# Kernel optimization log

Measured on AMD Instinct MI355X. Metric: run time of the kernel, lower is better.

## Reference

```python
import jax, jax.numpy as jnp
import numpy as np


def _ln(x, g, b, eps=1e-6):
    m = jnp.mean(x, axis=-1, keepdims=True)
    v = jnp.var(x, axis=-1, keepdims=True)
    return (x - m) * jax.lax.rsqrt(v + eps) * g + b


def setup_inputs():
    key = jax.random.key(0)
    ks = jax.random.split(key, 16)
    B, Hs, Ws, D = 2, 48, 48, 768
    heads, P = 6, 4
    L = Hs * Ws                # feat tokens (single level, 1/16 scale)
    N = 21 * (Hs * Ws // 4)    # query tokens: 16n + 4n + n multi-scale layout
    hidden = int(D * 0.25)
    s = 0.02
    return {
        "query": jax.random.normal(ks[0], (B, N, D), jnp.float32),
        "reference_points": jax.random.uniform(ks[1], (B, N, 1, 2), jnp.float32),
        "feat": jax.random.normal(ks[2], (B, L, D), jnp.float32),
        "spatial_shapes": jnp.array([[Hs, Ws]], jnp.int32),
        "level_start_index": jnp.array([0], jnp.int32),
        "H": Hs, "W": Ws,
        "qn_g": jnp.ones((D,), jnp.float32), "qn_b": jnp.zeros((D,), jnp.float32),
        "fn_g": jnp.ones((D,), jnp.float32), "fn_b": jnp.zeros((D,), jnp.float32),
        "Wv": jax.random.normal(ks[3], (D, D), jnp.float32) * s, "bv": jnp.zeros((D,), jnp.float32),
        "Woff": jax.random.normal(ks[4], (D, heads * P * 2), jnp.float32) * s,
        "boff": jax.random.normal(ks[5], (heads * P * 2,), jnp.float32) * s,
        "Wattn": jax.random.normal(ks[6], (D, heads * P), jnp.float32) * s,
        "battn": jnp.zeros((heads * P,), jnp.float32),
        "Wo": jax.random.normal(ks[7], (D, D), jnp.float32) * s, "bo": jnp.zeros((D,), jnp.float32),
        "ffn_g": jnp.ones((D,), jnp.float32), "ffn_b": jnp.zeros((D,), jnp.float32),
        "W1": jax.random.normal(ks[8], (D, hidden), jnp.float32) * s, "b1": jnp.zeros((hidden,), jnp.float32),
        "dw_w": jax.random.normal(ks[9], (hidden, 1, 3, 3), jnp.float32) * s, "dw_b": jnp.zeros((hidden,), jnp.float32),
        "W2": jax.random.normal(ks[10], (hidden, D), jnp.float32) * s, "b2": jnp.zeros((D,), jnp.float32),
    }


def reference(query, reference_points, feat, spatial_shapes, level_start_index, H, W,
              qn_g, qn_b, fn_g, fn_b, Wv, bv, Woff, boff, Wattn, battn, Wo, bo,
              ffn_g, ffn_b, W1, b1, dw_w, dw_b, W2, b2):
    B, N, D = query.shape
    heads, P = 6, 4
    dh = D // heads
    hidden = W1.shape[1]
    # ---- MSDeformAttn (single level) ----
    qn = _ln(query, qn_g, qn_b)
    fn = _ln(feat, fn_g, fn_b)
    value = (fn @ Wv + bv).reshape(B, -1, heads, dh)           # (B,L,h,dh)
    off = (qn @ Woff + boff).reshape(B, N, heads, 1, P, 2)
    aw = jax.nn.softmax((qn @ Wattn + battn).reshape(B, N, heads, P), axis=-1)
    # offset normalizer = [W_l, H_l]
    norm = jnp.stack([spatial_shapes[..., 1], spatial_shapes[..., 0]], -1).astype(qn.dtype)
    loc = reference_points[:, :, None, :, None, :] + off / norm[None, None, None, :, None, :]
    loc = loc[:, :, :, 0]  # (B,N,heads,P,2) single level
    # grid_sample bilinear, align_corners=False, zero padding
    x = loc[..., 0] * W - 0.5
    y = loc[..., 1] * H - 0.5
    x0 = jnp.floor(x); y0 = jnp.floor(y)
    wx = x - x0; wy = y - y0
    x0 = x0.astype(jnp.int32); y0 = y0.astype(jnp.int32)
    value_t = value.transpose(0, 2, 1, 3)  # (B,heads,L,dh)

    def corner(xi, yi, w):
        valid = (xi >= 0) & (xi < W) & (yi >= 0) & (yi < H)
        idx = jnp.clip(yi, 0, H - 1) * W + jnp.clip(xi, 0, W - 1)
        idx = idx.transpose(0, 2, 1, 3).reshape(B, heads, N * P)
        v = jnp.take_along_axis(value_t, idx[..., None], axis=2)  # (B,h,N*P,dh)
        wm = jnp.where(valid, w, 0.0).transpose(0, 2, 1, 3).reshape(B, heads, N * P)
        return v * wm[..., None]

    sampled = (corner(x0, y0, (1 - wx) * (1 - wy)) + corner(x0 + 1, y0, wx * (1 - wy))
               + corner(x0, y0 + 1, (1 - wx) * wy) + corner(x0 + 1, y0 + 1, wx * wy))
    sampled = sampled.reshape(B, heads, N, P, dh)
    attn = jnp.einsum('bhnpd,bnhp->bnhd', sampled, aw).reshape(B, N, D) @ Wo + bo
    query = query + attn
    # ---- ConvFFN (hidden=dim*cffn_ratio, multi-scale DWConv) ----
    h = _ln(query, ffn_g, ffn_b) @ W1 + b1
    n = N // 21

    def dw(t, hh, ww):
        img = t.transpose(0, 2, 1).reshape(B, hidden, hh, ww)
        out = jax.lax.conv_general_dilated(img, dw_w, (1, 1), 'SAME', feature_group_count=hidden)
        return (out + dw_b[None, :, None, None]).reshape(B, hidden, hh * ww).transpose(0, 2, 1)

    h = jnp.concatenate([dw(h[:, :16 * n], 2 * H, 2 * W),
                         dw(h[:, 16 * n:20 * n], H, W),
                         dw(h[:, 20 * n:], H // 2, W // 2)], axis=1)
    h = jax.nn.gelu(h, approximate=False)
    return query + (h @ W2 + b2)
```

## Files before the change

### kernel.cpp

```cpp
#include <hip/hip_runtime.h>
#include <math.h>

#define BB 2
#define NN 12096
#define LL 2304
#define DD 768
#define HID 192
#define HS 48
#define WS 48

typedef unsigned short u16;
typedef unsigned int u32;
typedef __attribute__((ext_vector_type(8))) __bf16 bf16x8;
typedef __attribute__((ext_vector_type(4))) float f32x4;

__device__ __forceinline__ u16 f2bf(float f) {
  u32 x = __builtin_bit_cast(u32, f);
  u32 r = (x + 0x7fffu + ((x >> 16) & 1u)) >> 16;
  return (u16)r;
}
__device__ __forceinline__ float bf2f(u16 u) {
  u32 x = ((u32)u) << 16;
  return __builtin_bit_cast(float, x);
}

template <typename T>
__device__ __forceinline__ void ln_row4(const T* xr, const float* g, const float* bta, u16* yr, int t) {
  float v0, v1, v2, v3;
  if constexpr (sizeof(T) == 2) {
    ushort4 u = *(const ushort4*)(xr + 4 * t);
    v0 = bf2f(u.x); v1 = bf2f(u.y); v2 = bf2f(u.z); v3 = bf2f(u.w);
  } else {
    float4 f = *(const float4*)(xr + 4 * t);
    v0 = f.x; v1 = f.y; v2 = f.z; v3 = f.w;
  }
  float s = v0 + v1 + v2 + v3;
  float s2 = v0 * v0 + v1 * v1 + v2 * v2 + v3 * v3;
#pragma unroll
  for (int off = 32; off; off >>= 1) {
    s += __shfl_down(s, off, 64);
    s2 += __shfl_down(s2, off, 64);
  }
  __shared__ float red[6];
  __shared__ float mv[2];
  int wave = t >> 6, lane = t & 63;
  if (lane == 0) { red[wave] = s; red[3 + wave] = s2; }
  __syncthreads();
  if (t == 0) {
    float ts = red[0] + red[1] + red[2];
    float ts2 = red[3] + red[4] + red[5];
    float m = ts * (1.f / DD);
    float var = ts2 * (1.f / DD) - m * m;
    mv[0] = m;
    mv[1] = rsqrtf(var + 1e-6f);
  }
  __syncthreads();
  float m = mv[0], rs = mv[1];
  float4 gv = *(const float4*)(g + 4 * t);
  float4 bv = *(const float4*)(bta + 4 * t);
  ushort4 o;
  o.x = f2bf((v0 - m) * rs * gv.x + bv.x);
  o.y = f2bf((v1 - m) * rs * gv.y + bv.y);
  o.z = f2bf((v2 - m) * rs * gv.z + bv.z);
  o.w = f2bf((v3 - m) * rs * gv.w + bv.w);
  *(ushort4*)(yr + 4 * t) = o;
}

template <typename T>
__global__ __launch_bounds__(192) void ln_kernel(const T* __restrict__ x,
                                                 const float* __restrict__ g,
                                                 const float* __restrict__ bta,
                                                 u16* __restrict__ y) {
  size_t row = blockIdx.x;
  ln_row4<T>(x + row * DD, g, bta, y + row * DD, threadIdx.x);
}

__global__ __launch_bounds__(192) void ln_dual_kernel(const float* __restrict__ xq,
                                                      const float* __restrict__ gq,
                                                      const float* __restrict__ bq,
                                                      u16* __restrict__ yq,
                                                      const float* __restrict__ xf,
                                                      const float* __restrict__ gf,
                                                      const float* __restrict__ bf_,
                                                      u16* __restrict__ yf,
                                                      int Mq) {
  size_t row = blockIdx.x;
  if (row < (size_t)Mq)
    ln_row4<float>(xq + row * DD, gq, bq, yq + row * DD, threadIdx.x);
  else {
    size_t r = row - Mq;
    ln_row4<float>(xf + r * DD, gf, bf_, yf + r * DD, threadIdx.x);
  }
}

template <int BM, int BN, int WM, int WN, int RES, int OUT, int NTSW>
__global__ __launch_bounds__(256, 4) void gemm_bf16(const u16* __restrict__ A,
                                                    const u16* __restrict__ Bt,
                                                    const float* __restrict__ bias,
                                                    const void* __restrict__ res,
                                                    void* __restrict__ Cv,
                                                    int M, int N, int K) {
  constexpr int PM = BM / WM, PN = BN / WN;
  constexpr int FM = PM / 16, FN = PN / 16;
  constexpr int ASEG = BM / 32;
  constexpr int BSEG = BN / 32;
  int bx, by;
  if (NTSW > 0) {
    int flat = blockIdx.x;
    int x = flat & 7, gidx = flat >> 3;
    bx = gidx % NTSW;
    int mg = gidx / NTSW;
    by = mg * 8 + x;
    if (by * BM >= M) return;
  } else {
    bx = blockIdx.x;
    by = blockIdx.y;
  }
  __shared__ u16 As[BM * 64];
  __shared__ u16 Bs[BN * 64];
  int tid = threadIdx.x;
  int w = tid >> 6, lane = tid & 63;
  int rw = w / WN, cw = w % WN;
  int m0 = by * BM, n0 = bx * BN;

  f32x4 acc[FM][FN];
#pragma unroll
  for (int i = 0; i < FM; ++i)
#pragma unroll
    for (int j = 0; j < FN; ++j) acc[i][j] = (f32x4){0.f, 0.f, 0.f, 0.f};

  int lr = lane >> 3;
  int lq = lane & 7;
  int qg = lq ^ lr;
  int l15 = lane & 15, quad = lane >> 4;

  for (int k0 = 0; k0 < K; k0 += 64) {
#pragma unroll
    for (int i = 0; i < ASEG; ++i) {
      int s = w * ASEG + i;
      int row = s * 8 + lr;
      const u16* gp = A + (size_t)(m0 + row) * K + k0 + qg * 8;
      __builtin_amdgcn_global_load_lds(
          (const __attribute__((address_space(1))) void*)gp,
          (__attribute__((address_space(3))) void*)&As[s * 512], 16, 0, 0);
    }
#pragma unroll
    for (int i = 0; i < BSEG; ++i) {
      int s = w * BSEG + i;
      int row = s * 8 + lr;
      const u16* gp = Bt + (size_t)(n0 + row) * K + k0 + qg * 8;
      __builtin_amdgcn_global_load_lds(
          (const __attribute__((address_space(1))) void*)gp,
          (__attribute__((address_space(3))) void*)&Bs[s * 512], 16, 0, 0);
    }
    __syncthreads();
#pragma unroll
    for (int s2 = 0; s2 < 2; ++s2) {
      bf16x8 af[FM], bfr[FN];
#pragma unroll
      for (int mt = 0; mt < FM; ++mt) {
        int rm = rw * PM + mt * 16 + l15;
        int ch = (s2 * 4 + quad) ^ (rm & 7);
        af[mt] = *(const bf16x8*)&As[rm * 64 + ch * 8];
      }
#pragma unroll
      for (int nt = 0; nt < FN; ++nt) {
        int rn = cw * PN + nt * 16 + l15;
        int ch = (s2 * 4 + quad) ^ (rn & 7);
        bfr[nt] = *(const bf16x8*)&Bs[rn * 64 + ch * 8];
      }
#pragma unroll
      for (int mt = 0; mt < FM; ++mt)
#pragma unroll
        for (int nt = 0; nt < FN; ++nt)
          acc[mt][nt] = __builtin_amdgcn_mfma_f32_16x16x32_bf16(af[mt], bfr[nt], acc[mt][nt], 0, 0, 0);
    }
    __syncthreads();
  }

#pragma unroll
  for (int mt = 0; mt < FM; ++mt) {
    int m = m0 + rw * PM + mt * 16 + quad * 4;
#pragma unroll
    for (int nt = 0; nt < FN; ++nt) {
      int n = n0 + cw * PN + nt * 16 + l15;
      float bsv = bias[n];
#pragma unroll
      for (int r = 0; r < 4; ++r) {
        size_t idx = (size_t)(m + r) * N + n;
        float v = acc[mt][nt][r] + bsv;
        if (RES == 1) v += ((const float*)res)[idx];
        if (RES == 2) v += bf2f(((const u16*)res)[idx]);
        if (OUT == 1) ((u16*)Cv)[idx] = f2bf(v);
        else ((float*)Cv)[idx] = v;
      }
    }
  }
}

#define PREP_B0 (DD * DD)
#define PREP_B1 (2 * DD * DD)
#define PREP_B2 (PREP_B1 + HID * DD)
#define PREP_B3 (PREP_B2 + HID * DD)
#define PREP_B4 (PREP_B3 + 128 * DD)
__global__ __launch_bounds__(256) void prep_all(const float* __restrict__ Wv, const float* __restrict__ Wo,
                                                const float* __restrict__ W1, const float* __restrict__ W2,
                                                const float* __restrict__ Woff, const float* __restrict__ Wattn,
                                                const float* __restrict__ boff, const float* __restrict__ battn,
                                                u16* __restrict__ Wv_t, u16* __restrict__ Wo_t,
                                                u16* __restrict__ W1_t, u16* __restrict__ W2_t,
                                                u16* __restrict__ Wcat_t, float* __restrict__ bias_cat) {
  int idx = blockIdx.x * 256 + threadIdx.x;
  if (idx >= PREP_B4) return;
  if (idx < PREP_B0) {
    int n = idx / DD, k = idx - n * DD;
    Wv_t[idx] = f2bf(Wv[(size_t)k * DD + n]);
  } else if (idx < PREP_B1) {
    int l = idx - PREP_B0;
    int n = l / DD, k = l - n * DD;
    Wo_t[l] = f2bf(Wo[(size_t)k * DD + n]);
  } else if (idx < PREP_B2) {
    int l = idx - PREP_B1;
    int n = l / DD, k = l - n * DD;
    W1_t[l] = f2bf(W1[(size_t)k * HID + n]);
  } else if (idx < PREP_B3) {
    int l = idx - PREP_B2;
    int n = l / HID, k = l - n * HID;
    W2_t[l] = f2bf(W2[(size_t)k * DD + n]);
  } else {
    int l = idx - PREP_B3;
    int n = l / DD, k = l - n * DD;
    float v = 0.f;
    if (n < 48) v = Woff[(size_t)k * 48 + n];
    else if (n < 72) v = Wattn[(size_t)k * 24 + (n - 48)];
    Wcat_t[l] = f2bf(v);
    if (l < 128) {
      float b = 0.f;
      if (l < 48) b = boff[l];
      else if (l < 72) b = battn[l - 48];
      bias_cat[l] = b;
    }
  }
}

__global__ __launch_bounds__(192) void sample_kernel(const u16* __restrict__ value,
                                                     const float* __restrict__ off,
                                                     const float* __restrict__ refp,
                                                     u16* __restrict__ s) {
  int flat = blockIdx.x;
  int b = flat & 1;
  size_t row = (size_t)b * NN + (flat >> 1);
  __shared__ int cidx[96];
  __shared__ float cw[96];
  int t = threadIdx.x;
  if (t < 24) {
    const float* o = off + row * 128;
    int hh = t >> 2, p = t & 3;
    float l0 = o[48 + hh * 4 + 0], l1 = o[48 + hh * 4 + 1];
    float l2 = o[48 + hh * 4 + 2], l3 = o[48 + hh * 4 + 3];
    float mx = fmaxf(fmaxf(l0, l1), fmaxf(l2, l3));
    float e0 = expf(l0 - mx), e1 = expf(l1 - mx), e2 = expf(l2 - mx), e3 = expf(l3 - mx);
    float sum = e0 + e1 + e2 + e3;
    float et = (p == 0) ? e0 : (p == 1) ? e1 : (p == 2) ? e2 : e3;
    float aw = et / sum;
    float x = refp[row * 2 + 0] * (float)WS - 0.5f + o[hh * 8 + p * 2 + 0];
    float y = refp[row * 2 + 1] * (float)HS - 0.5f + o[hh * 8 + p * 2 + 1];
    float xf = floorf(x), yf = floorf(y);
    int x0 = (int)xf, y0 = (int)yf;
    float wx = x - xf, wy = y - yf;
#pragma unroll
    for (int c = 0; c < 4; ++c) {
      int xi = x0 + (c & 1), yi = y0 + (c >> 1);
      float w = ((c & 1) ? wx : 1.f - wx) * ((c >> 1) ? wy : 1.f - wy);
      bool valid = (xi >= 0) && (xi < WS) && (yi >= 0) && (yi < HS);
      int xc = min(max(xi, 0), WS - 1), yc = min(max(yi, 0), HS - 1);
      cidx[t * 4 + c] = yc * WS + xc;
      cw[t * 4 + c] = valid ? w * aw : 0.f;
    }
  }
  __syncthreads();
  const u16* vb = value + (size_t)b * LL * DD;
  int c = t * 4;
  int h = c >> 7;
  int base0 = h * 16;
  ushort4 v[16];
#pragma unroll
  for (int i = 0; i < 16; ++i)
    v[i] = *(const ushort4*)&vb[(size_t)cidx[base0 + i] * DD + c];
  float a0 = 0.f, a1 = 0.f, a2 = 0.f, a3 = 0.f;
#pragma unroll
  for (int i = 0; i < 16; ++i) {
    float w = cw[base0 + i];
    a0 += w * bf2f(v[i].x);
    a1 += w * bf2f(v[i].y);
    a2 += w * bf2f(v[i].z);
    a3 += w * bf2f(v[i].w);
  }
  ushort4 o4;
  o4.x = f2bf(a0); o4.y = f2bf(a1); o4.z = f2bf(a2); o4.w = f2bf(a3);
  *(ushort4*)&s[row * DD + c] = o4;
}

__global__ __launch_bounds__(256) void dwconv_gelu_kernel(const u16* __restrict__ h,
                                                          const float* __restrict__ w,
                                                          const float* __restrict__ bias,
                                                          u16* __restrict__ out) {
  size_t idx = (size_t)blockIdx.x * 256 + threadIdx.x;
  if (idx >= (size_t)BB * NN * (HID / 4)) return;
  int c4 = (int)(idx % (HID / 4));
  int c = c4 * 4;
  int rem = (int)(idx / (HID / 4));
  int nidx = rem % NN;
  int b = rem / NN;
  int hh, ww, base;
  if (nidx < 9216)       { hh = 96; ww = 96; base = 0; }
  else if (nidx < 11520) { hh = 48; ww = 48; base = 9216; }
  else                   { hh = 24; ww = 24; base = 11520; }
  int p = nidx - base;
  int y = p / ww, x = p % ww;
  const u16* hb = h + ((size_t)b * NN + base) * HID;
  float a0 = bias[c], a1 = bias[c + 1], a2 = bias[c + 2], a3 = bias[c + 3];
#pragma unroll
  for (int dy = -1; dy <= 1; ++dy) {
    int yy = y + dy;
    if (yy < 0 || yy >= hh) continue;
#pragma unroll
    for (int dx = -1; dx <= 1; ++dx) {
      int xx = x + dx;
      if (xx < 0 || xx >= ww) continue;
      ushort4 v = *(const ushort4*)&hb[((size_t)(yy * ww + xx)) * HID + c];
      int k = (dy + 1) * 3 + (dx + 1);
      a0 += bf2f(v.x) * w[(c + 0) * 9 + k];
      a1 += bf2f(v.y) * w[(c + 1) * 9 + k];
      a2 += bf2f(v.z) * w[(c + 2) * 9 + k];
      a3 += bf2f(v.w) * w[(c + 3) * 9 + k];
    }
  }
  ushort4 o;
  o.x = f2bf(0.5f * a0 * (1.f + erff(a0 * 0.70710678118654752f)));
  o.y = f2bf(0.5f * a1 * (1.f + erff(a1 * 0.70710678118654752f)));
  o.z = f2bf(0.5f * a2 * (1.f + erff(a2 * 0.70710678118654752f)));
  o.w = f2bf(0.5f * a3 * (1.f + erff(a3 * 0.70710678118654752f)));
  *(ushort4*)&out[(size_t)rem * HID + c] = o;
}

extern "C" void kernel_launch(void* const* d_in, const int* in_sizes, int n_in,
                              void* d_out, int out_size, void* d_ws, size_t ws_size,
                              hipStream_t stream) {
  const float* query = (const float*)d_in[0];
  const float* refp  = (const float*)d_in[1];
  const float* feat  = (const float*)d_in[2];
  const float* qn_g  = (const float*)d_in[7];
  const float* qn_b  = (const float*)d_in[8];
  const float* fn_g  = (const float*)d_in[9];
  const float* fn_b  = (const float*)d_in[10];
  const float* Wv    = (const float*)d_in[11];
  const float* bv    = (const float*)d_in[12];
  const float* Woff  = (const float*)d_in[13];
  const float* boff  = (const float*)d_in[14];
  const float* Wattn = (const float*)d_in[15];
  const float* battn = (const float*)d_in[16];
  const float* Wo    = (const float*)d_in[17];
  const float* bo    = (const float*)d_in[18];
  const float* ffn_g = (const float*)d_in[19];
  const float* ffn_b = (const float*)d_in[20];
  const float* W1    = (const float*)d_in[21];
  const float* b1    = (const float*)d_in[22];
  const float* dw_w  = (const float*)d_in[23];
  const float* dw_b  = (const float*)d_in[24];
  const float* W2    = (const float*)d_in[25];
  const float* b2    = (const float*)d_in[26];
  float* out = (float*)d_out;

  const int Mq = BB * NN;
  const int Mf = BB * LL;

  char* p = (char*)d_ws;
  auto alloc = [&](size_t bytes) { char* r = p; p += (bytes + 255) & ~(size_t)255; return r; };
  u16* qn_bf   = (u16*)alloc((size_t)Mq * DD * 2);
  u16* fn_bf   = (u16*)alloc((size_t)Mf * DD * 2);
  u16* val_bf  = (u16*)alloc((size_t)Mf * DD * 2);
  float* off   = (float*)alloc((size_t)Mq * 128 * 4);
  u16* s_bf    = (u16*)alloc((size_t)Mq * DD * 2);
  u16* q2_bf   = (u16*)alloc((size_t)Mq * DD * 2);
  u16* h_bf    = (u16*)alloc((size_t)Mq * HID * 2);
  u16* h2_bf   = (u16*)alloc((size_t)Mq * HID * 2);
  u16* Wv_t    = (u16*)alloc((size_t)DD * DD * 2);
  u16* Wo_t    = (u16*)alloc((size_t)DD * DD * 2);
  u16* W1_t    = (u16*)alloc((size_t)HID * DD * 2);
  u16* W2_t    = (u16*)alloc((size_t)DD * HID * 2);
  u16* Wcat_t  = (u16*)alloc((size_t)128 * DD * 2);
  float* bias_cat = (float*)alloc(128 * 4);

  prep_all<<<(PREP_B4 + 255) / 256, 256, 0, stream>>>(Wv, Wo, W1, W2, Woff, Wattn, boff, battn,
                                                      Wv_t, Wo_t, W1_t, W2_t, Wcat_t, bias_cat);

  ln_dual_kernel<<<Mq + Mf, 192, 0, stream>>>(query, qn_g, qn_b, qn_bf, feat, fn_g, fn_b, fn_bf, Mq);

  gemm_bf16<128, 64, 2, 2, 0, 1, 12><<<((Mf / 128 + 7) / 8) * 8 * 12, 256, 0, stream>>>(
      fn_bf, Wv_t, bv, nullptr, val_bf, Mf, DD, DD);

  gemm_bf16<64, 64, 2, 2, 0, 0, 2><<<((Mq / 64 + 7) / 8) * 8 * 2, 256, 0, stream>>>(
      qn_bf, Wcat_t, bias_cat, nullptr, off, Mq, 128, DD);

  sample_kernel<<<Mq, 192, 0, stream>>>(val_bf, off, refp, s_bf);

  gemm_bf16<128, 64, 2, 2, 1, 1, 12><<<((Mq / 128 + 7) / 8) * 8 * 12, 256, 0, stream>>>(
      s_bf, Wo_t, bo, query, q2_bf, Mq, DD, DD);

  ln_kernel<u16><<<Mq, 192, 0, stream>>>(q2_bf, ffn_g, ffn_b, qn_bf);

  gemm_bf16<32, 192, 1, 4, 0, 1, 0><<<dim3(1, Mq / 32), 256, 0, stream>>>(
      qn_bf, W1_t, b1, nullptr, h_bf, Mq, HID, DD);

  {
    size_t total = (size_t)BB * NN * (HID / 4);
    int blocks = (int)((total + 255) / 256);
    dwconv_gelu_kernel<<<blocks, 256, 0, stream>>>(h_bf, dw_w, dw_b, h2_bf);
  }

  gemm_bf16<128, 64, 2, 2, 2, 0, 12><<<((Mq / 128 + 7) / 8) * 8 * 12, 256, 0, stream>>>(
      h2_bf, W2_t, b2, q2_bf, out, Mq, DD, HID);
}
```

Baseline: 408.2 us.

## Double-buffer LDS tiles in bf16 GEMM to overlap global loads with MFMA

Adds a DBUF template option that keeps two LDS buffers per operand. The kernel prefetches the next K-tile with global_load_lds while the current one is computed, using explicit vmcnt waits and raw s_barrier instead of __syncthreads. This is meant to hide global-to-LDS latency in the main GEMMs. It doubles LDS use and lowers the occupancy hint from 4 to 3 blocks, and the hand-written waitcnt/barrier sequencing depends on per-thread load counts being correct.

```diff
diff --git a/kernel.cpp b/kernel.cpp
--- a/kernel.cpp
+++ b/kernel.cpp
@@ -22,6 +22,16 @@
 __device__ __forceinline__ float bf2f(u16 u) {
   u32 x = ((u32)u) << 16;
   return __builtin_bit_cast(float, x);
+}
+
+template <int N>
+__device__ __forceinline__ void waitcnt_vm() {
+  if constexpr (N == 0)       asm volatile("s_waitcnt vmcnt(0)" ::: "memory");
+  else if constexpr (N == 2)  asm volatile("s_waitcnt vmcnt(2)" ::: "memory");
+  else if constexpr (N == 4)  asm volatile("s_waitcnt vmcnt(4)" ::: "memory");
+  else if constexpr (N == 6)  asm volatile("s_waitcnt vmcnt(6)" ::: "memory");
+  else if constexpr (N == 8)  asm volatile("s_waitcnt vmcnt(8)" ::: "memory");
+  else                        asm volatile("s_waitcnt vmcnt(12)" ::: "memory");
 }
 
 template <typename T>
@@ -93,8 +103,8 @@
   }
 }
 
-template <int BM, int BN, int WM, int WN, int RES, int OUT, int NTSW>
-__global__ __launch_bounds__(256, 4) void gemm_bf16(const u16* __restrict__ A,
+template <int BM, int BN, int WM, int WN, int RES, int OUT, int NTSW, int DBUF>
+__global__ __launch_bounds__(256, (DBUF ? 3 : 4)) void gemm_bf16(const u16* __restrict__ A,
                                                     const u16* __restrict__ Bt,
                                                     const float* __restrict__ bias,
                                                     const void* __restrict__ res,
@@ -104,6 +114,7 @@
   constexpr int FM = PM / 16, FN = PN / 16;
   constexpr int ASEG = BM / 32;
   constexpr int BSEG = BN / 32;
+  constexpr int LPT = ASEG + BSEG;
   int bx, by;
   if (NTSW > 0) {
     int flat = blockIdx.x;
@@ -116,8 +127,8 @@
     bx = blockIdx.x;
     by = blockIdx.y;
   }
-  __shared__ u16 As[BM * 64];
-  __shared__ u16 Bs[BN * 64];
+  __shared__ u16 As[(1 + DBUF) * BM * 64];
+  __shared__ u16 Bs[(1 + DBUF) * BN * 64];
   int tid = threadIdx.x;
   int w = tid >> 6, lane = tid & 63;
   int rw = w / WN, cw = w % WN;
@@ -134,26 +145,30 @@
   int qg = lq ^ lr;
   int l15 = lane & 15, quad = lane >> 4;
 
-  for (int k0 = 0; k0 < K; k0 += 64) {
+  int nk = K >> 6;
+
+  auto stage = [&](int kk, int buf) {
 #pragma unroll
     for (int i = 0; i < ASEG; ++i) {
       int s = w * ASEG + i;
       int row = s * 8 + lr;
-      const u16* gp = A + (size_t)(m0 + row) * K + k0 + qg * 8;
+      const u16* gp = A + (size_t)(m0 + row) * K + kk * 64 + qg * 8;
       __builtin_amdgcn_global_load_lds(
           (const __attribute__((address_space(1))) void*)gp,
-          (__attribute__((address_space(3))) void*)&As[s * 512], 16, 0, 0);
+          (__attribute__((address_space(3))) void*)&As[buf * (BM * 64) + s * 512], 16, 0, 0);
     }
 #pragma unroll
     for (int i = 0; i < BSEG; ++i) {
       int s = w * BSEG + i;
       int row = s * 8 + lr;
-      const u16* gp = Bt + (size_t)(n0 + row) * K + k0 + qg * 8;
+      const u16* gp = Bt + (size_t)(n0 + row) * K + kk * 64 + qg * 8;
       __builtin_amdgcn_global_load_lds(
           (const __attribute__((address_space(1))) void*)gp,
-          (__attribute__((address_space(3))) void*)&Bs[s * 512], 16, 0, 0);
-    }
-    __syncthreads();
+          (__attribute__((address_space(3))) void*)&Bs[buf * (BN * 64) + s * 512], 16, 0, 0);
+    }
+  };
+
+  auto compute = [&](const u16* Ab, const u16* Bb) {
 #pragma unroll
     for (int s2 = 0; s2 < 2; ++s2) {
       bf16x8 af[FM], bfr[FN];
@@ -161,13 +176,13 @@
       for (int mt = 0; mt < FM; ++mt) {
         int rm = rw * PM + mt * 16 + l15;
         int ch = (s2 * 4 + quad) ^ (rm & 7);
-        af[mt] = *(const bf16x8*)&As[rm * 64 + ch * 8];
+        af[mt] = *(const bf16x8*)&Ab[rm * 64 + ch * 8];
       }
 #pragma unroll
       for (int nt = 0; nt < FN; ++nt) {
         int rn = cw * PN + nt * 16 + l15;
         int ch = (s2 * 4 + quad) ^ (rn & 7);
-        bfr[nt] = *(const bf16x8*)&Bs[rn * 64 + ch * 8];
+        bfr[nt] = *(const bf16x8*)&Bb[rn * 64 + ch * 8];
       }
 #pragma unroll
       for (int mt = 0; mt < FM; ++mt)
@@ -175,7 +190,29 @@
         for (int nt = 0; nt < FN; ++nt)
           acc[mt][nt] = __builtin_amdgcn_mfma_f32_16x16x32_bf16(af[mt], bfr[nt], acc[mt][nt], 0, 0, 0);
     }
-    __syncthreads();
+  };
+
+  if (DBUF == 0) {
+    for (int t = 0; t < nk; ++t) {
+      stage(t, 0);
+      __syncthreads();
+      compute(As, Bs);
+      __syncthreads();
+    }
+  } else {
+    stage(0, 0);
+    for (int t = 0; t < nk; ++t) {
+      int cur = t & 1;
+      if (t + 1 < nk) {
+        stage(t + 1, cur ^ 1);
+        waitcnt_vm<LPT>();
+      } else {
+        waitcnt_vm<0>();
+      }
+      __builtin_amdgcn_s_barrier();
+      compute(&As[cur * (BM * 64)], &Bs[cur * (BN * 64)]);
+      if (t + 1 < nk) __builtin_amdgcn_s_barrier();
+    }
   }
 
 #pragma unroll
@@ -397,20 +434,20 @@
 
   ln_dual_kernel<<<Mq + Mf, 192, 0, stream>>>(query, qn_g, qn_b, qn_bf, feat, fn_g, fn_b, fn_bf, Mq);
 
-  gemm_bf16<128, 64, 2, 2, 0, 1, 12><<<((Mf / 128 + 7) / 8) * 8 * 12, 256, 0, stream>>>(
+  gemm_bf16<128, 64, 2, 2, 0, 1, 12, 1><<<((Mf / 128 + 7) / 8) * 8 * 12, 256, 0, stream>>>(
       fn_bf, Wv_t, bv, nullptr, val_bf, Mf, DD, DD);
 
-  gemm_bf16<64, 64, 2, 2, 0, 0, 2><<<((Mq / 64 + 7) / 8) * 8 * 2, 256, 0, stream>>>(
+  gemm_bf16<64, 64, 2, 2, 0, 0, 2, 1><<<((Mq / 64 + 7) / 8) * 8 * 2, 256, 0, stream>>>(
       qn_bf, Wcat_t, bias_cat, nullptr, off, Mq, 128, DD);
 
   sample_kernel<<<Mq, 192, 0, stream>>>(val_bf, off, refp, s_bf);
 
-  gemm_bf16<128, 64, 2, 2, 1, 1, 12><<<((Mq / 128 + 7) / 8) * 8 * 12, 256, 0, stream>>>(
+  gemm_bf16<128, 64, 2, 2, 1, 1, 12, 1><<<((Mq / 128 + 7) / 8) * 8 * 12, 256, 0, stream>>>(
       s_bf, Wo_t, bo, query, q2_bf, Mq, DD, DD);
 
   ln_kernel<u16><<<Mq, 192, 0, stream>>>(q2_bf, ffn_g, ffn_b, qn_bf);
 
-  gemm_bf16<32, 192, 1, 4, 0, 1, 0><<<dim3(1, Mq / 32), 256, 0, stream>>>(
+  gemm_bf16<32, 192, 1, 4, 0, 1, 0, 0><<<dim3(1, Mq / 32), 256, 0, stream>>>(
       qn_bf, W1_t, b1, nullptr, h_bf, Mq, HID, DD);
 
   {
@@ -419,6 +456,6 @@
     dwconv_gelu_kernel<<<blocks, 256, 0, stream>>>(h_bf, dw_w, dw_b, h2_bf);
   }
 
-  gemm_bf16<128, 64, 2, 2, 2, 0, 12><<<((Mq / 128 + 7) / 8) * 8 * 12, 256, 0, stream>>>(
+  gemm_bf16<128, 64, 2, 2, 2, 0, 12, 1><<<((Mq / 128 + 7) / 8) * 8 * 12, 256, 0, stream>>>(
       h2_bf, W2_t, b2, q2_bf, out, Mq, DD, HID);
 }
```

New measurement: 413.7 us. No clear change (+1.3%).
